# Kernel tuning notes

Measured on AMD Instinct MI355X. Metric: run time of the kernel, lower is better.

Reference implementation:

```python
import jax, jax.numpy as jnp
import numpy as np

N_NODES = 50000
N_EDGES = 800000
D_IN = 128
D_HID = 128


def gcn_conv(x, W, b, src, dst, ew, n_nodes):
    """PyG GCNConv: add self-loops (weight 1), symmetric deg^-1/2 normalization,
    aggregate messages from src at dst, then h = Ahat x W + b."""
    # linear transform first (PyG applies lin before propagate)
    h = x @ W  # [N, D_out]
    loops = jnp.arange(n_nodes, dtype=src.dtype)
    s = jnp.concatenate([src, loops])
    d = jnp.concatenate([dst, loops])
    w = jnp.concatenate([ew, jnp.ones((n_nodes,), dtype=ew.dtype)])
    deg = jax.ops.segment_sum(w, d, num_segments=n_nodes)  # [N]
    dinv = jnp.where(deg > 0, jax.lax.rsqrt(deg), 0.0)
    norm = dinv[s] * w * dinv[d]  # [E+N]
    msg = norm[:, None] * h[s]  # [E+N, D_out]
    out = jax.ops.segment_sum(msg, d, num_segments=n_nodes)
    return out + b


def setup_inputs() -> dict:
    key = jax.random.key(0)
    k1, k2, k3, k4, k5 = jax.random.split(key, 5)
    x = jax.random.normal(k1, (N_NODES, D_IN), dtype=jnp.float32)
    edge_index = jax.random.randint(k2, (2, N_EDGES), 0, N_NODES, dtype=jnp.int64)
    edge_weight = jax.random.uniform(k3, (N_EDGES,), dtype=jnp.float32)
    # glorot-style init for GCN layer weights
    s1 = 1.0 / np.sqrt(D_IN)
    s2 = 1.0 / np.sqrt(D_HID)
    W1 = jax.random.uniform(k4, (D_IN, D_HID), minval=-s1, maxval=s1, dtype=jnp.float32)
    W2 = jax.random.uniform(k5, (D_HID, D_HID), minval=-s2, maxval=s2, dtype=jnp.float32)
    b1 = jnp.zeros((D_HID,), dtype=jnp.float32)
    b2 = jnp.zeros((D_HID,), dtype=jnp.float32)
    return {"x": x, "edge_index": edge_index, "edge_weight": edge_weight,
            "W1": W1, "b1": b1, "W2": W2, "b2": b2}


def reference(x, edge_index, edge_weight, W1, b1, W2, b2):
    n = x.shape[0]
    src, dst = edge_index[0], edge_index[1]
    x1 = jax.nn.relu(gcn_conv(x, W1, b1, src, dst, edge_weight, n))
    x2 = jax.nn.relu(gcn_conv(x1, W2, b2, src, dst, edge_weight, n))
    return jnp.concatenate([x1[:, :, None], x2[:, :, None]], axis=2)  # [N, D_HID, 2]
```

## Files before the change

### kernel.cpp

```cpp
#include <hip/hip_runtime.h>

#define NN 50000
#define NE 800000
#define D 128
#define SCAN_CH 1024
#define SCAN_NB ((NN + SCAN_CH - 1) / SCAN_CH)

typedef __attribute__((ext_vector_type(8))) short short8;
typedef __attribute__((ext_vector_type(4))) float f32x4;
typedef unsigned short ushort;
typedef unsigned int uint;
typedef unsigned long long u64;

__device__ inline ushort f2b(float x) {
    uint u = __float_as_uint(x);
    return (ushort)((u + 0x7fffu + ((u >> 16) & 1u)) >> 16);
}
__device__ inline float blo(uint u) { return __uint_as_float(u << 16); }
__device__ inline float bhi(uint u) { return __uint_as_float(u & 0xffff0000u); }


__global__ __launch_bounds__(256) void k_init(u64* __restrict__ pc, int n) {
    int i = blockIdx.x * 256 + threadIdx.x;
    if (i < n) pc[i] = 0ull;
}


__global__ __launch_bounds__(256) void k_wt(const float* __restrict__ W1,
                                            const float* __restrict__ W2,
                                            ushort* __restrict__ wtb1,
                                            ushort* __restrict__ wtb2) {
    int g = blockIdx.x * 256 + threadIdx.x;
    const float* W = (g < D * D) ? W1 : W2;
    ushort* wt = (g < D * D) ? wtb1 : wtb2;
    int idx = (g < D * D) ? g : g - D * D;
    if (g < 2 * D * D) {
        int k = idx >> 7, c = idx & 127;
        wt[c * D + k] = f2b(W[idx]);
    }
}


__global__ __launch_bounds__(256) void k_deg_cnt(const int* __restrict__ dst,
                                                 const float* __restrict__ ew,
                                                 u64* __restrict__ pc,
                                                 int* __restrict__ erank, int e) {
    int i = blockIdx.x * 256 + threadIdx.x;
    if (i < e) {
        int d = dst[i];
        uint fx = (uint)(ew[i] * 16777216.0f + 0.5f);
        u64 pack = (1ull << 32) | (u64)fx;
        u64 old = atomicAdd(&pc[d], pack);
        erank[i] = (int)(old >> 32);
    }
}


__global__ __launch_bounds__(256) void k_scan_part(const u64* __restrict__ pc,
                                                   int* __restrict__ blockSums,
                                                   float* __restrict__ rsd, int n) {
    __shared__ int s[256];
    const int tid = threadIdx.x;
    const int base = blockIdx.x * SCAN_CH + tid * 4;
    int c0 = 0, c1 = 0, c2 = 0, c3 = 0;
    const float sc = 1.0f / 16777216.0f;
    if (base + 3 < n) {
        u64 p0 = pc[base + 0], p1 = pc[base + 1], p2 = pc[base + 2], p3 = pc[base + 3];
        c0 = (int)(p0 >> 32); c1 = (int)(p1 >> 32);
        c2 = (int)(p2 >> 32); c3 = (int)(p3 >> 32);
        float4 dv;
        dv.x = rsqrtf(1.0f + (float)(uint)p0 * sc);
        dv.y = rsqrtf(1.0f + (float)(uint)p1 * sc);
        dv.z = rsqrtf(1.0f + (float)(uint)p2 * sc);
        dv.w = rsqrtf(1.0f + (float)(uint)p3 * sc);
        *(float4*)&rsd[base] = dv;
    } else {
        for (int j = 0; j < 4; ++j) {
            if (base + j < n) {
                u64 p = pc[base + j];
                int cj = (int)(p >> 32);
                if (j == 0) c0 = cj; else if (j == 1) c1 = cj; else if (j == 2) c2 = cj; else c3 = cj;
                rsd[base + j] = rsqrtf(1.0f + (float)(uint)p * sc);
            }
        }
    }
    s[tid] = c0 + c1 + c2 + c3;
    __syncthreads();
    for (int off = 1; off < 256; off <<= 1) {
        int v = s[tid];
        int add = (tid >= off) ? s[tid - off] : 0;
        __syncthreads();
        s[tid] = v + add;
        __syncthreads();
    }
    if (tid == 255) blockSums[blockIdx.x] = s[255];
}

__global__ __launch_bounds__(64) void k_scan_mid(const int* __restrict__ blockSums,
                                                 int* __restrict__ blockOffs, int nb) {
    int l = threadIdx.x;
    int v = (l < nb) ? blockSums[l] : 0;
    int inc = v;
#pragma unroll
    for (int off = 1; off < 64; off <<= 1) {
        int u = __shfl_up(inc, off);
        if (l >= off) inc += u;
    }
    if (l < nb) blockOffs[l] = inc - v;
}

__global__ __launch_bounds__(256) void k_scan_add(const u64* __restrict__ pc,
                                                  const int* __restrict__ blockOffs,
                                                  int* __restrict__ rowptr, int n, int e) {
    __shared__ int s[256];
    const int tid = threadIdx.x;
    const int base = blockIdx.x * SCAN_CH + tid * 4;
    int c0 = 0, c1 = 0, c2 = 0, c3 = 0;
    if (base + 3 < n) {
        c0 = (int)(pc[base + 0] >> 32); c1 = (int)(pc[base + 1] >> 32);
        c2 = (int)(pc[base + 2] >> 32); c3 = (int)(pc[base + 3] >> 32);
    } else {
        if (base + 0 < n) c0 = (int)(pc[base + 0] >> 32);
        if (base + 1 < n) c1 = (int)(pc[base + 1] >> 32);
        if (base + 2 < n) c2 = (int)(pc[base + 2] >> 32);
    }
    int tsum = c0 + c1 + c2 + c3;
    s[tid] = tsum;
    __syncthreads();
    for (int off = 1; off < 256; off <<= 1) {
        int v = s[tid];
        int add = (tid >= off) ? s[tid - off] : 0;
        __syncthreads();
        s[tid] = v + add;
        __syncthreads();
    }
    int p = blockOffs[blockIdx.x] + s[tid] - tsum;
    int p0 = p, p1 = p + c0, p2 = p + c0 + c1, p3 = p + c0 + c1 + c2;
    if (base + 3 < n) {
        *(int4*)&rowptr[base] = make_int4(p0, p1, p2, p3);
    } else {
        if (base + 0 < n) rowptr[base + 0] = p0;
        if (base + 1 < n) rowptr[base + 1] = p1;
        if (base + 2 < n) rowptr[base + 2] = p2;
    }
    if (blockIdx.x == 0 && tid == 0) rowptr[n] = e;
}


__global__ __launch_bounds__(256) void k_scatter(const int* __restrict__ src,
                                                 const int* __restrict__ dst,
                                                 const float* __restrict__ ew,
                                                 const float* __restrict__ rsd,
                                                 const int* __restrict__ rowptr,
                                                 const int* __restrict__ erank,
                                                 int2* __restrict__ edges, int e) {
    int i = blockIdx.x * 256 + threadIdx.x;
    if (i >= e) return;
    int s = src[i];
    int d = dst[i];
    float nrm = rsd[s] * ew[i] * rsd[d];
    int pos = rowptr[d] + erank[i];
    int2 ev;
    ev.x = s;
    ev.y = __float_as_int(nrm);
    edges[pos] = ev;
}


__global__ __launch_bounds__(256) void k_gemm(const float* __restrict__ A,
                                              const ushort* __restrict__ wtb,
                                              ushort* __restrict__ h, int n) {
    __shared__ ushort bounce[4][16][136];
    const int w = threadIdx.x >> 6, l = threadIdx.x & 63;
    const int r = l & 15, hg = l >> 4;
    const int node = blockIdx.x * 64 + w * 16 + r;
    const bool valid = node < n;
    const float* arow = A + (size_t)(valid ? node : 0) * D;

    short8 afr[4];
#pragma unroll
    for (int kk = 0; kk < 4; ++kk) {
        float4 p = *(const float4*)(arow + kk * 32 + hg * 8);
        float4 q = *(const float4*)(arow + kk * 32 + hg * 8 + 4);
        short8 t;
        t[0] = (short)f2b(p.x); t[1] = (short)f2b(p.y);
        t[2] = (short)f2b(p.z); t[3] = (short)f2b(p.w);
        t[4] = (short)f2b(q.x); t[5] = (short)f2b(q.y);
        t[6] = (short)f2b(q.z); t[7] = (short)f2b(q.w);
        afr[kk] = t;
    }

#pragma unroll
    for (int ct = 0; ct < 8; ++ct) {
        f32x4 acc = {0.f, 0.f, 0.f, 0.f};
#pragma unroll
        for (int kk = 0; kk < 4; ++kk) {
            short8 b = *(const short8*)(wtb + (size_t)(ct * 16 + r) * D + kk * 32 + hg * 8);
            acc = __builtin_amdgcn_mfma_f32_16x16x32_bf16(afr[kk], b, acc, 0, 0, 0);
        }
#pragma unroll
        for (int g = 0; g < 4; ++g)
            bounce[w][hg * 4 + g][ct * 16 + r] = f2b(acc[g]);
    }
    __syncthreads();

#pragma unroll
    for (int it = 0; it < 4; ++it) {
        int cid = it * 64 + l;
        int nl = cid >> 4;
        int ch = cid & 15;
        int onode = blockIdx.x * 64 + w * 16 + nl;
        if (onode < n) {
            int4 vv = *(const int4*)&bounce[w][nl][ch * 8];
            *(int4*)(h + (size_t)onode * D + ch * 8) = vv;
        }
    }
}


#define AGG_BODY                                                               \
    float rv = rsd[v];                                                         \
    float dinv2 = rv * rv;                                                     \
    uint us = *(const uint*)(hb + (size_t)v * D + f);                          \
    float accx = dinv2 * blo(us);                                              \
    float accy = dinv2 * bhi(us);                                              \
    int beg = rowptr[v], end = rowptr[v + 1];                                  \
    for (int base = beg; base < end; base += 64) {                             \
        int idx = base + lane;                                                 \
        int2 ev = (idx < end) ? edges[idx] : make_int2(v, 0);                  \
        int mm = min(64, end - base);                                          \
        for (int sb = 0; sb < 4; ++sb) {                                       \
            if (sb * 16 >= mm) break;                                          \
            uint u[16];                                                        \
            float ws[16];                                                      \
            _Pragma("unroll")                                                  \
            for (int j = 0; j < 16; ++j) {                                     \
                int s = __builtin_amdgcn_readlane(ev.x, sb * 16 + j);          \
                ws[j] = __uint_as_float((uint)__builtin_amdgcn_readlane(ev.y, sb * 16 + j)); \
                u[j] = *(const uint*)(hb + (size_t)s * D + f);                 \
            }                                                                  \
            _Pragma("unroll")                                                  \
            for (int j = 0; j < 16; ++j) {                                     \
                accx += ws[j] * blo(u[j]);                                     \
                accy += ws[j] * bhi(u[j]);                                     \
            }                                                                  \
        }                                                                      \
    }

__global__ __launch_bounds__(256) void k_agg1(const int* __restrict__ rowptr,
                                              const int2* __restrict__ edges,
                                              const float* __restrict__ rsd,
                                              const ushort* __restrict__ hb,
                                              const float* __restrict__ b,
                                              float* __restrict__ x1, int n) {
    int v = (blockIdx.x * 256 + threadIdx.x) >> 6;
    if (v >= n) return;
    int lane = threadIdx.x & 63;
    int f = lane * 2;
    AGG_BODY
    float2 o;
    o.x = fmaxf(accx + b[f + 0], 0.0f);
    o.y = fmaxf(accy + b[f + 1], 0.0f);
    *(float2*)&x1[(size_t)v * D + f] = o;
}

__global__ __launch_bounds__(256) void k_agg2(const int* __restrict__ rowptr,
                                              const int2* __restrict__ edges,
                                              const float* __restrict__ rsd,
                                              const ushort* __restrict__ hb,
                                              const float* __restrict__ x1,
                                              const float* __restrict__ b,
                                              float* __restrict__ out, int n) {
    int v = (blockIdx.x * 256 + threadIdx.x) >> 6;
    if (v >= n) return;
    int lane = threadIdx.x & 63;
    int f = lane * 2;
    AGG_BODY
    float2 xv = *(const float2*)&x1[(size_t)v * D + f];
    float4 o;
    o.x = xv.x;
    o.y = fmaxf(accx + b[f + 0], 0.0f);
    o.z = xv.y;
    o.w = fmaxf(accy + b[f + 1], 0.0f);
    *(float4*)&out[((size_t)v * D + f) * 2] = o;
}

extern "C" void kernel_launch(void* const* d_in, const int* in_sizes, int n_in,
                              void* d_out, int out_size, void* d_ws, size_t ws_size,
                              hipStream_t stream) {
    const float* x  = (const float*)d_in[0];
    const int*   ei = (const int*)d_in[1];
    const float* ew = (const float*)d_in[2];
    const float* W1 = (const float*)d_in[3];
    const float* b1 = (const float*)d_in[4];
    const float* W2 = (const float*)d_in[5];
    const float* b2 = (const float*)d_in[6];
    float* out = (float*)d_out;

    const int* src = ei;
    const int* dst = ei + NE;

    char* w = (char*)d_ws;
    auto take = [&](size_t bytes) {
        char* p = w;
        w += (bytes + 255) & ~(size_t)255;
        return p;
    };
    u64*    pc        = (u64*)take((size_t)NN * 8);
    float*  rsd       = (float*)take((size_t)NN * 4);
    int*    rowptr    = (int*)take((size_t)(NN + 1) * 4);
    int*    blockSums = (int*)take((size_t)SCAN_NB * 4);
    int*    blockOffs = (int*)take((size_t)SCAN_NB * 4);
    int*    erank     = (int*)take((size_t)NE * 4);
    int2*   edges     = (int2*)take((size_t)NE * 8);
    ushort* wtb1      = (ushort*)take((size_t)D * D * 2);
    ushort* wtb2      = (ushort*)take((size_t)D * D * 2);
    ushort* hb        = (ushort*)take((size_t)NN * D * 2);
    float*  x1        = (float*)take((size_t)NN * D * 4);

    const int nBlkN   = (NN + 255) / 256;
    const int nBlkE   = (NE + 255) / 256;
    const int nBlkG   = (NN + 63) / 64;
    const int nBlkAgg = (NN * 64 + 255) / 256;
    const int nBlkW   = (2 * D * D + 255) / 256;

    k_wt<<<nBlkW, 256, 0, stream>>>(W1, W2, wtb1, wtb2);
    k_init<<<nBlkN, 256, 0, stream>>>(pc, NN);
    k_deg_cnt<<<nBlkE, 256, 0, stream>>>(dst, ew, pc, erank, NE);
    k_scan_part<<<SCAN_NB, 256, 0, stream>>>(pc, blockSums, rsd, NN);
    k_scan_mid<<<1, 64, 0, stream>>>(blockSums, blockOffs, SCAN_NB);
    k_scan_add<<<SCAN_NB, 256, 0, stream>>>(pc, blockOffs, rowptr, NN, NE);
    k_scatter<<<nBlkE, 256, 0, stream>>>(src, dst, ew, rsd, rowptr, erank, edges, NE);

    k_gemm<<<nBlkG, 256, 0, stream>>>(x, wtb1, hb, NN);
    k_agg1<<<nBlkAgg, 256, 0, stream>>>(rowptr, edges, rsd, hb, b1, x1, NN);

    k_gemm<<<nBlkG, 256, 0, stream>>>(x1, wtb2, hb, NN);
    k_agg2<<<nBlkAgg, 256, 0, stream>>>(rowptr, edges, rsd, hb, x1, b2, out, NN);
}
```

Before: 263.6 us.

## Fold degree normalization into GEMM epilogue and merge setup kernels

Moves the source-side deg^-1/2 scaling into the GEMM output (h scaled per row) and the destination-side scaling into the aggregation epilogue, so edges store raw weights and the scatter no longer does random rsd gathers. It also fuses the init and weight-transpose kernels, folds the mid-level scan into k_scan_add, and vectorizes the degree-count kernel to four edges per thread. This removes several launches and per-edge random reads, at the cost of redundant 64-lane scans in every scan_add block and a slightly different bf16 rounding point.

```diff
diff --git a/kernel.cpp b/kernel.cpp
--- a/kernel.cpp
+++ b/kernel.cpp
@@ -20,21 +20,17 @@
 __device__ inline float bhi(uint u) { return __uint_as_float(u & 0xffff0000u); }
 
 
-__global__ __launch_bounds__(256) void k_init(u64* __restrict__ pc, int n) {
-    int i = blockIdx.x * 256 + threadIdx.x;
-    if (i < n) pc[i] = 0ull;
-}
-
-
-__global__ __launch_bounds__(256) void k_wt(const float* __restrict__ W1,
-                                            const float* __restrict__ W2,
-                                            ushort* __restrict__ wtb1,
-                                            ushort* __restrict__ wtb2) {
+__global__ __launch_bounds__(256) void k_init_wt(u64* __restrict__ pc,
+                                                 const float* __restrict__ W1,
+                                                 const float* __restrict__ W2,
+                                                 ushort* __restrict__ wtb1,
+                                                 ushort* __restrict__ wtb2, int n) {
     int g = blockIdx.x * 256 + threadIdx.x;
-    const float* W = (g < D * D) ? W1 : W2;
-    ushort* wt = (g < D * D) ? wtb1 : wtb2;
-    int idx = (g < D * D) ? g : g - D * D;
+    if (g < n) pc[g] = 0ull;
     if (g < 2 * D * D) {
+        const float* W = (g < D * D) ? W1 : W2;
+        ushort* wt = (g < D * D) ? wtb1 : wtb2;
+        int idx = (g < D * D) ? g : g - D * D;
         int k = idx >> 7, c = idx & 127;
         wt[c * D + k] = f2b(W[idx]);
     }
@@ -44,15 +40,29 @@
 __global__ __launch_bounds__(256) void k_deg_cnt(const int* __restrict__ dst,
                                                  const float* __restrict__ ew,
                                                  u64* __restrict__ pc,
-                                                 int* __restrict__ erank, int e) {
+                                                 int* __restrict__ erank, int e4) {
     int i = blockIdx.x * 256 + threadIdx.x;
-    if (i < e) {
-        int d = dst[i];
-        uint fx = (uint)(ew[i] * 16777216.0f + 0.5f);
-        u64 pack = (1ull << 32) | (u64)fx;
-        u64 old = atomicAdd(&pc[d], pack);
-        erank[i] = (int)(old >> 32);
-    }
+    if (i >= e4) return;
+    int4 d4 = *(const int4*)&dst[i * 4];
+    float4 w4 = *(const float4*)&ew[i * 4];
+    int4 r4;
+    {
+        uint fx = (uint)(w4.x * 16777216.0f + 0.5f);
+        r4.x = (int)(atomicAdd(&pc[d4.x], (1ull << 32) | (u64)fx) >> 32);
+    }
+    {
+        uint fx = (uint)(w4.y * 16777216.0f + 0.5f);
+        r4.y = (int)(atomicAdd(&pc[d4.y], (1ull << 32) | (u64)fx) >> 32);
+    }
+    {
+        uint fx = (uint)(w4.z * 16777216.0f + 0.5f);
+        r4.z = (int)(atomicAdd(&pc[d4.z], (1ull << 32) | (u64)fx) >> 32);
+    }
+    {
+        uint fx = (uint)(w4.w * 16777216.0f + 0.5f);
+        r4.w = (int)(atomicAdd(&pc[d4.w], (1ull << 32) | (u64)fx) >> 32);
+    }
+    *(int4*)&erank[i * 4] = r4;
 }
 
 
@@ -96,24 +106,23 @@
     if (tid == 255) blockSums[blockIdx.x] = s[255];
 }
 
-__global__ __launch_bounds__(64) void k_scan_mid(const int* __restrict__ blockSums,
-                                                 int* __restrict__ blockOffs, int nb) {
-    int l = threadIdx.x;
-    int v = (l < nb) ? blockSums[l] : 0;
-    int inc = v;
-#pragma unroll
-    for (int off = 1; off < 64; off <<= 1) {
-        int u = __shfl_up(inc, off);
-        if (l >= off) inc += u;
-    }
-    if (l < nb) blockOffs[l] = inc - v;
-}
 
 __global__ __launch_bounds__(256) void k_scan_add(const u64* __restrict__ pc,
-                                                  const int* __restrict__ blockOffs,
+                                                  const int* __restrict__ blockSums,
                                                   int* __restrict__ rowptr, int n, int e) {
     __shared__ int s[256];
+    __shared__ int s_boff;
     const int tid = threadIdx.x;
+    if (tid < 64) {
+        int v = (tid < SCAN_NB) ? blockSums[tid] : 0;
+        int inc = v;
+#pragma unroll
+        for (int off = 1; off < 64; off <<= 1) {
+            int u = __shfl_up(inc, off);
+            if (tid >= off) inc += u;
+        }
+        if (tid == blockIdx.x) s_boff = inc - v;
+    }
     const int base = blockIdx.x * SCAN_CH + tid * 4;
     int c0 = 0, c1 = 0, c2 = 0, c3 = 0;
     if (base + 3 < n) {
@@ -134,7 +143,7 @@
         s[tid] = v + add;
         __syncthreads();
     }
-    int p = blockOffs[blockIdx.x] + s[tid] - tsum;
+    int p = s_boff + s[tid] - tsum;
     int p0 = p, p1 = p + c0, p2 = p + c0 + c1, p3 = p + c0 + c1 + c2;
     if (base + 3 < n) {
         *(int4*)&rowptr[base] = make_int4(p0, p1, p2, p3);
@@ -150,25 +159,23 @@
 __global__ __launch_bounds__(256) void k_scatter(const int* __restrict__ src,
                                                  const int* __restrict__ dst,
                                                  const float* __restrict__ ew,
-                                                 const float* __restrict__ rsd,
                                                  const int* __restrict__ rowptr,
                                                  const int* __restrict__ erank,
                                                  int2* __restrict__ edges, int e) {
     int i = blockIdx.x * 256 + threadIdx.x;
     if (i >= e) return;
-    int s = src[i];
     int d = dst[i];
-    float nrm = rsd[s] * ew[i] * rsd[d];
     int pos = rowptr[d] + erank[i];
     int2 ev;
-    ev.x = s;
-    ev.y = __float_as_int(nrm);
+    ev.x = src[i];
+    ev.y = __float_as_int(ew[i]);
     edges[pos] = ev;
 }
 
 
 __global__ __launch_bounds__(256) void k_gemm(const float* __restrict__ A,
                                               const ushort* __restrict__ wtb,
+                                              const float* __restrict__ rsd,
                                               ushort* __restrict__ h, int n) {
     __shared__ ushort bounce[4][16][136];
     const int w = threadIdx.x >> 6, l = threadIdx.x & 63;
@@ -190,6 +197,13 @@
         afr[kk] = t;
     }
 
+    float rs[4];
+#pragma unroll
+    for (int g = 0; g < 4; ++g) {
+        int nd = blockIdx.x * 64 + w * 16 + hg * 4 + g;
+        rs[g] = (nd < n) ? rsd[nd] : 1.0f;
+    }
+
 #pragma unroll
     for (int ct = 0; ct < 8; ++ct) {
         f32x4 acc = {0.f, 0.f, 0.f, 0.f};
@@ -200,7 +214,7 @@
         }
 #pragma unroll
         for (int g = 0; g < 4; ++g)
-            bounce[w][hg * 4 + g][ct * 16 + r] = f2b(acc[g]);
+            bounce[w][hg * 4 + g][ct * 16 + r] = f2b(acc[g] * rs[g]);
     }
     __syncthreads();
 
@@ -220,10 +234,9 @@
 
 #define AGG_BODY                                                               \
     float rv = rsd[v];                                                         \
-    float dinv2 = rv * rv;                                                     \
     uint us = *(const uint*)(hb + (size_t)v * D + f);                          \
-    float accx = dinv2 * blo(us);                                              \
-    float accy = dinv2 * bhi(us);                                              \
+    float accx = blo(us);                                                      \
+    float accy = bhi(us);                                                      \
     int beg = rowptr[v], end = rowptr[v + 1];                                  \
     for (int base = beg; base < end; base += 64) {                             \
         int idx = base + lane;                                                 \
@@ -259,8 +272,8 @@
     int f = lane * 2;
     AGG_BODY
     float2 o;
-    o.x = fmaxf(accx + b[f + 0], 0.0f);
-    o.y = fmaxf(accy + b[f + 1], 0.0f);
+    o.x = fmaxf(rv * accx + b[f + 0], 0.0f);
+    o.y = fmaxf(rv * accy + b[f + 1], 0.0f);
     *(float2*)&x1[(size_t)v * D + f] = o;
 }
 
@@ -279,9 +292,9 @@
     float2 xv = *(const float2*)&x1[(size_t)v * D + f];
     float4 o;
     o.x = xv.x;
-    o.y = fmaxf(accx + b[f + 0], 0.0f);
+    o.y = fmaxf(rv * accx + b[f + 0], 0.0f);
     o.z = xv.y;
-    o.w = fmaxf(accy + b[f + 1], 0.0f);
+    o.w = fmaxf(rv * accy + b[f + 1], 0.0f);
     *(float4*)&out[((size_t)v * D + f) * 2] = o;
 }
 
@@ -310,7 +323,6 @@
     float*  rsd       = (float*)take((size_t)NN * 4);
     int*    rowptr    = (int*)take((size_t)(NN + 1) * 4);
     int*    blockSums = (int*)take((size_t)SCAN_NB * 4);
-    int*    blockOffs = (int*)take((size_t)SCAN_NB * 4);
     int*    erank     = (int*)take((size_t)NE * 4);
     int2*   edges     = (int2*)take((size_t)NE * 8);
     ushort* wtb1      = (ushort*)take((size_t)D * D * 2);
@@ -320,21 +332,19 @@
 
     const int nBlkN   = (NN + 255) / 256;
     const int nBlkE   = (NE + 255) / 256;
+    const int nBlkE4  = (NE / 4 + 255) / 256;
     const int nBlkG   = (NN + 63) / 64;
     const int nBlkAgg = (NN * 64 + 255) / 256;
-    const int nBlkW   = (2 * D * D + 255) / 256;
-
-    k_wt<<<nBlkW, 256, 0, stream>>>(W1, W2, wtb1, wtb2);
-    k_init<<<nBlkN, 256, 0, stream>>>(pc, NN);
-    k_deg_cnt<<<nBlkE, 256, 0, stream>>>(dst, ew, pc, erank, NE);
+
+    k_init_wt<<<nBlkN, 256, 0, stream>>>(pc, W1, W2, wtb1, wtb2, NN);
+    k_deg_cnt<<<nBlkE4, 256, 0, stream>>>(dst, ew, pc, erank, NE / 4);
     k_scan_part<<<SCAN_NB, 256, 0, stream>>>(pc, blockSums, rsd, NN);
-    k_scan_mid<<<1, 64, 0, stream>>>(blockSums, blockOffs, SCAN_NB);
-    k_scan_add<<<SCAN_NB, 256, 0, stream>>>(pc, blockOffs, rowptr, NN, NE);
-    k_scatter<<<nBlkE, 256, 0, stream>>>(src, dst, ew, rsd, rowptr, erank, edges, NE);
-
-    k_gemm<<<nBlkG, 256, 0, stream>>>(x, wtb1, hb, NN);
+    k_scan_add<<<SCAN_NB, 256, 0, stream>>>(pc, blockSums, rowptr, NN, NE);
+    k_scatter<<<nBlkE, 256, 0, stream>>>(src, dst, ew, rowptr, erank, edges, NE);
+
+    k_gemm<<<nBlkG, 256, 0, stream>>>(x, wtb1, rsd, hb, NN);
     k_agg1<<<nBlkAgg, 256, 0, stream>>>(rowptr, edges, rsd, hb, b1, x1, NN);
 
-    k_gemm<<<nBlkG, 256, 0, stream>>>(x1, wtb2, hb, NN);
+    k_gemm<<<nBlkG, 256, 0, stream>>>(x1, wtb2, rsd, hb, NN);
     k_agg2<<<nBlkAgg, 256, 0, stream>>>(rowptr, edges, rsd, hb, x1, b2, out, NN);
 }
```

Result: faster. 257.1 us (-2.5%).
